# Kernel tuning notes

Measured on AMD Instinct MI355X. Metric: run time of the kernel, lower is better.

Reference implementation:

```python
import jax, jax.numpy as jnp
import numpy as np

def setup_inputs() -> dict:
    key = jax.random.key(0)
    k1, k2 = jax.random.split(key)
    bb_feats = jax.random.normal(k1, (8, 512, 128, 128), dtype=jnp.float32)
    aux_out = jax.random.normal(k2, (8, 19, 128, 128), dtype=jnp.float32)
    return {"bb_feats": bb_feats, "aux_out": aux_out}

def reference(bb_feats, aux_out):
    B, K, H, W = aux_out.shape
    C = bb_feats.shape[1]
    probs = jax.nn.softmax(aux_out.reshape(B, K, H * W), axis=2)  # [B,K,HW]
    feats = bb_feats.reshape(B, C, H * W)                          # [B,C,HW]
    # weighted sum over spatial dim: [B,K,HW] x [B,C,HW] -> [B,K,C]
    ctx = jnp.einsum('bks,bcs->bkc', probs, feats)
    # -> [B,C,K,1]
    return jnp.transpose(ctx, (0, 2, 1))[..., None]
```

## Files before the change

### kernel.cpp

```cpp
#include <hip/hip_runtime.h>
#include <math.h>

#define B 8
#define C 512
#define K 19
#define HW 16384
#define ROWS (B * K)
#define L2E 1.44269504088896340736f

#define NSEG 8
#define SEG (HW / NSEG)

#define NW 4
#define CPW 4
#define CPB (CPW * NW)
#define CG (C / CPB)
#define NSC 4
#define SCHUNK (HW / NSC)
#define TS 256
#define NT (SCHUNK / TS)

__global__ __launch_bounds__(256)
void softmax_partial_kernel(const float* __restrict__ aux, float* __restrict__ partials) {
    int blk = blockIdx.x;
    int row = blk >> 3;
    int seg = blk & (NSEG - 1);
    const float4* x4 = (const float4*)(aux + (size_t)row * HW + seg * SEG);
    int tid  = threadIdx.x;
    int lane = tid & 63;
    int wave = tid >> 6;
    __shared__ float red[4];

    float4 v0 = x4[tid];
    float4 v1 = x4[tid + 256];
    float m = fmaxf(fmaxf(fmaxf(v0.x, v0.y), fmaxf(v0.z, v0.w)),
                    fmaxf(fmaxf(v1.x, v1.y), fmaxf(v1.z, v1.w)));
    #pragma unroll
    for (int off = 32; off > 0; off >>= 1) m = fmaxf(m, __shfl_xor(m, off, 64));
    if (lane == 0) red[wave] = m;
    __syncthreads();
    m = fmaxf(fmaxf(red[0], red[1]), fmaxf(red[2], red[3]));
    __syncthreads();

    float s = exp2f((v0.x - m) * L2E) + exp2f((v0.y - m) * L2E)
            + exp2f((v0.z - m) * L2E) + exp2f((v0.w - m) * L2E)
            + exp2f((v1.x - m) * L2E) + exp2f((v1.y - m) * L2E)
            + exp2f((v1.z - m) * L2E) + exp2f((v1.w - m) * L2E);
    #pragma unroll
    for (int off = 32; off > 0; off >>= 1) s += __shfl_xor(s, off, 64);
    if (lane == 0) red[wave] = s;
    __syncthreads();
    if (tid == 0) {
        partials[blk * 2]     = m;
        partials[blk * 2 + 1] = red[0] + red[1] + red[2] + red[3];
    }
}

__global__ __launch_bounds__(256)
void softmax_combine_kernel(const float* __restrict__ partials, float* __restrict__ stats) {
    int row = threadIdx.x;
    if (row < ROWS) {
        float mj[NSEG], zj[NSEG];
        float m = -INFINITY;
        #pragma unroll
        for (int j = 0; j < NSEG; j++) {
            mj[j] = partials[(row * NSEG + j) * 2];
            zj[j] = partials[(row * NSEG + j) * 2 + 1];
            m = fmaxf(m, mj[j]);
        }
        float Z = 0.f;
        #pragma unroll
        for (int j = 0; j < NSEG; j++) Z += zj[j] * exp2f((mj[j] - m) * L2E);
        stats[row * 2]     = -m * L2E;
        stats[row * 2 + 1] = 1.0f / Z;
    }
}

__global__ __launch_bounds__(256)
__attribute__((amdgpu_waves_per_eu(2)))
void gather_kernel(const float* __restrict__ feats, const float* __restrict__ aux,
                   const float* __restrict__ stats, float* __restrict__ out) {
    __shared__ float plds[2][K][TS];

    int bid  = blockIdx.x;
    int sc   = bid & (NSC - 1);
    int cg   = (bid >> 2) & (CG - 1);
    int b    = bid >> 7;
    int tid  = threadIdx.x;
    int lane = tid & 63;
    int wave = tid >> 6;
    int c0   = cg * CPB + wave * CPW;

    const float* Abase = aux   + (size_t)b * K * HW + sc * SCHUNK;
    const float* Fbase = feats + ((size_t)b * C + c0) * HW + sc * SCHUNK;
    const float* S     = stats + (size_t)b * K * 2;

    float negml[K], invz[K];
    #pragma unroll
    for (int k = 0; k < K; k++) {
        negml[k] = __int_as_float(__builtin_amdgcn_readfirstlane(__float_as_int(S[2 * k])));
        invz[k]  = __int_as_float(__builtin_amdgcn_readfirstlane(__float_as_int(S[2 * k + 1])));
    }

    float acc[CPW][K];
    #pragma unroll
    for (int c = 0; c < CPW; c++)
        #pragma unroll
        for (int k = 0; k < K; k++) acc[c][k] = 0.f;

    #pragma unroll
    for (int k = 0; k < K; k++) {
        float a = Abase[k * HW + tid];
        plds[0][k][tid] = exp2f(fmaf(a, L2E, negml[k])) * invz[k];
    }
    float4 f_cur[CPW], f_next[CPW];
    #pragma unroll
    for (int c = 0; c < CPW; c++)
        f_cur[c] = *(const float4*)(Fbase + c * HW + lane * 4);

    for (int t = 0; t < NT; t++) {
        int buf = t & 1;
        __syncthreads();

        if (t + 1 < NT) {
            int s1 = (t + 1) * TS;
            #pragma unroll
            for (int c = 0; c < CPW; c++)
                f_next[c] = *(const float4*)(Fbase + c * HW + s1 + lane * 4);
            #pragma unroll
            for (int kb = 0; kb < K; kb += 5) {
                float a[5];
                const int ke = (kb + 5 < K) ? kb + 5 : K;
                #pragma unroll
                for (int k = kb; k < ke; k++) a[k - kb] = Abase[k * HW + s1 + tid];
                #pragma unroll
                for (int k = kb; k < ke; k++)
                    plds[buf ^ 1][k][tid] = exp2f(fmaf(a[k - kb], L2E, negml[k])) * invz[k];
            }
        }

        #pragma unroll
        for (int k = 0; k < K; k++) {
            float4 p4 = *(const float4*)(&plds[buf][k][lane * 4]);
            #pragma unroll
            for (int c = 0; c < CPW; c++) {
                acc[c][k] = fmaf(p4.x, f_cur[c].x, acc[c][k]);
                acc[c][k] = fmaf(p4.y, f_cur[c].y, acc[c][k]);
                acc[c][k] = fmaf(p4.z, f_cur[c].z, acc[c][k]);
                acc[c][k] = fmaf(p4.w, f_cur[c].w, acc[c][k]);
            }
        }
        #pragma unroll
        for (int c = 0; c < CPW; c++) f_cur[c] = f_next[c];
    }

    #pragma unroll
    for (int c = 0; c < CPW; c++)
        #pragma unroll
        for (int k = 0; k < K; k++) {
            float v = acc[c][k];
            #pragma unroll
            for (int off = 32; off > 0; off >>= 1) v += __shfl_xor(v, off, 64);
            if (lane == 0)
                atomicAdd(&out[((size_t)b * C + c0 + c) * K + k], v);
        }
}

extern "C" void kernel_launch(void* const* d_in, const int* in_sizes, int n_in,
                              void* d_out, int out_size, void* d_ws, size_t ws_size,
                              hipStream_t stream) {
    const float* feats = (const float*)d_in[0];
    const float* aux   = (const float*)d_in[1];
    float* out      = (float*)d_out;
    float* stats    = (float*)d_ws;
    float* partials = (float*)d_ws + 512;

    hipMemsetAsync(d_out, 0, (size_t)out_size * sizeof(float), stream);
    softmax_partial_kernel<<<ROWS * NSEG, 256, 0, stream>>>(aux, partials);
    softmax_combine_kernel<<<1, 256, 0, stream>>>(partials, stats);
    gather_kernel<<<B * CG * NSC, 256, 0, stream>>>(feats, aux, stats, out);
}
```

Before: 407.2 us.

## Materialize softmax probabilities once and stream them into LDS via direct loads

Replaces the two-stage softmax statistics kernels with one kernel per row that writes fully normalized probabilities to workspace. The gather kernel then loads those probabilities straight into LDS with global_load_lds, which removes the per-block exp recomputation that was repeated for every channel group. It also remaps block IDs so that blocks sharing the same batch and spatial chunk land on the same XCD, aiming for better L2 reuse. In exchange, the probability tensor makes an extra write and read round trip through memory, and the 1024-thread single-row blocks launch only 152 blocks.

Measured after the change: 395.0 us. 3.0% less time.

```diff
diff --git a/kernel.cpp b/kernel.cpp
--- a/kernel.cpp
+++ b/kernel.cpp
@@ -8,9 +8,6 @@
 #define ROWS (B * K)
 #define L2E 1.44269504088896340736f
 
-#define NSEG 8
-#define SEG (HW / NSEG)
-
 #define NW 4
 #define CPW 4
 #define CPB (CPW * NW)
@@ -20,87 +17,85 @@
 #define TS 256
 #define NT (SCHUNK / TS)
 
-__global__ __launch_bounds__(256)
-void softmax_partial_kernel(const float* __restrict__ aux, float* __restrict__ partials) {
-    int blk = blockIdx.x;
-    int row = blk >> 3;
-    int seg = blk & (NSEG - 1);
-    const float4* x4 = (const float4*)(aux + (size_t)row * HW + seg * SEG);
+typedef __attribute__((address_space(3))) unsigned int lds_u32;
+typedef const __attribute__((address_space(1))) unsigned int glb_u32;
+
+__global__ __launch_bounds__(1024)
+void probs_kernel(const float* __restrict__ aux, float* __restrict__ probs) {
+    int row  = blockIdx.x;
     int tid  = threadIdx.x;
     int lane = tid & 63;
     int wave = tid >> 6;
-    __shared__ float red[4];
+    __shared__ float red[16];
 
-    float4 v0 = x4[tid];
-    float4 v1 = x4[tid + 256];
-    float m = fmaxf(fmaxf(fmaxf(v0.x, v0.y), fmaxf(v0.z, v0.w)),
-                    fmaxf(fmaxf(v1.x, v1.y), fmaxf(v1.z, v1.w)));
+    const float4* x4 = (const float4*)(aux + (size_t)row * HW);
+    float4*       p4 = (float4*)(probs + (size_t)row * HW);
+
+    float4 v[4];
+    #pragma unroll
+    for (int i = 0; i < 4; i++) v[i] = x4[tid + i * 1024];
+
+    float m = -INFINITY;
+    #pragma unroll
+    for (int i = 0; i < 4; i++)
+        m = fmaxf(m, fmaxf(fmaxf(v[i].x, v[i].y), fmaxf(v[i].z, v[i].w)));
     #pragma unroll
     for (int off = 32; off > 0; off >>= 1) m = fmaxf(m, __shfl_xor(m, off, 64));
     if (lane == 0) red[wave] = m;
     __syncthreads();
-    m = fmaxf(fmaxf(red[0], red[1]), fmaxf(red[2], red[3]));
+    #pragma unroll
+    for (int w = 0; w < 16; w++) m = fmaxf(m, red[w]);
     __syncthreads();
 
-    float s = exp2f((v0.x - m) * L2E) + exp2f((v0.y - m) * L2E)
-            + exp2f((v0.z - m) * L2E) + exp2f((v0.w - m) * L2E)
-            + exp2f((v1.x - m) * L2E) + exp2f((v1.y - m) * L2E)
-            + exp2f((v1.z - m) * L2E) + exp2f((v1.w - m) * L2E);
+    float nm = -m * L2E;
+    float s = 0.f;
+    #pragma unroll
+    for (int i = 0; i < 4; i++) {
+        v[i].x = exp2f(fmaf(v[i].x, L2E, nm));
+        v[i].y = exp2f(fmaf(v[i].y, L2E, nm));
+        v[i].z = exp2f(fmaf(v[i].z, L2E, nm));
+        v[i].w = exp2f(fmaf(v[i].w, L2E, nm));
+        s += (v[i].x + v[i].y) + (v[i].z + v[i].w);
+    }
     #pragma unroll
     for (int off = 32; off > 0; off >>= 1) s += __shfl_xor(s, off, 64);
     if (lane == 0) red[wave] = s;
     __syncthreads();
-    if (tid == 0) {
-        partials[blk * 2]     = m;
-        partials[blk * 2 + 1] = red[0] + red[1] + red[2] + red[3];
-    }
-}
+    float Z = 0.f;
+    #pragma unroll
+    for (int w = 0; w < 16; w++) Z += red[w];
+    float inv = 1.0f / Z;
 
-__global__ __launch_bounds__(256)
-void softmax_combine_kernel(const float* __restrict__ partials, float* __restrict__ stats) {
-    int row = threadIdx.x;
-    if (row < ROWS) {
-        float mj[NSEG], zj[NSEG];
-        float m = -INFINITY;
-        #pragma unroll
-        for (int j = 0; j < NSEG; j++) {
-            mj[j] = partials[(row * NSEG + j) * 2];
-            zj[j] = partials[(row * NSEG + j) * 2 + 1];
-            m = fmaxf(m, mj[j]);
-        }
-        float Z = 0.f;
-        #pragma unroll
-        for (int j = 0; j < NSEG; j++) Z += zj[j] * exp2f((mj[j] - m) * L2E);
-        stats[row * 2]     = -m * L2E;
-        stats[row * 2 + 1] = 1.0f / Z;
+    #pragma unroll
+    for (int i = 0; i < 4; i++) {
+        float4 o;
+        o.x = v[i].x * inv; o.y = v[i].y * inv;
+        o.z = v[i].z * inv; o.w = v[i].w * inv;
+        p4[tid + i * 1024] = o;
     }
 }
 
 __global__ __launch_bounds__(256)
 __attribute__((amdgpu_waves_per_eu(2)))
-void gather_kernel(const float* __restrict__ feats, const float* __restrict__ aux,
-                   const float* __restrict__ stats, float* __restrict__ out) {
+void gather_kernel(const float* __restrict__ feats, const float* __restrict__ probs,
+                   float* __restrict__ out) {
     __shared__ float plds[2][K][TS];
 
-    int bid  = blockIdx.x;
-    int sc   = bid & (NSC - 1);
-    int cg   = (bid >> 2) & (CG - 1);
-    int b    = bid >> 7;
+    int bid = blockIdx.x;
+    int xcd = bid & 7;
+    int lid = xcd * 128 + (bid >> 3);
+    int cg  = lid & (CG - 1);
+    int grp = lid >> 5;
+    int sc  = grp & (NSC - 1);
+    int b   = grp >> 2;
+
     int tid  = threadIdx.x;
     int lane = tid & 63;
     int wave = tid >> 6;
     int c0   = cg * CPB + wave * CPW;
 
-    const float* Abase = aux   + (size_t)b * K * HW + sc * SCHUNK;
+    const float* Pbase = probs + (size_t)b * K * HW + sc * SCHUNK;
     const float* Fbase = feats + ((size_t)b * C + c0) * HW + sc * SCHUNK;
-    const float* S     = stats + (size_t)b * K * 2;
-
-    float negml[K], invz[K];
-    #pragma unroll
-    for (int k = 0; k < K; k++) {
-        negml[k] = __int_as_float(__builtin_amdgcn_readfirstlane(__float_as_int(S[2 * k])));
-        invz[k]  = __int_as_float(__builtin_amdgcn_readfirstlane(__float_as_int(S[2 * k + 1])));
-    }
 
     float acc[CPW][K];
     #pragma unroll
@@ -108,11 +103,9 @@
         #pragma unroll
         for (int k = 0; k < K; k++) acc[c][k] = 0.f;
 
-    #pragma unroll
-    for (int k = 0; k < K; k++) {
-        float a = Abase[k * HW + tid];
-        plds[0][k][tid] = exp2f(fmaf(a, L2E, negml[k])) * invz[k];
-    }
+    for (int k = wave; k < K; k += NW)
+        __builtin_amdgcn_global_load_lds((glb_u32*)(Pbase + (size_t)k * HW + lane * 4),
+                                         (lds_u32*)&plds[0][k][0], 16, 0, 0);
     float4 f_cur[CPW], f_next[CPW];
     #pragma unroll
     for (int c = 0; c < CPW; c++)
@@ -127,27 +120,20 @@
             #pragma unroll
             for (int c = 0; c < CPW; c++)
                 f_next[c] = *(const float4*)(Fbase + c * HW + s1 + lane * 4);
-            #pragma unroll
-            for (int kb = 0; kb < K; kb += 5) {
-                float a[5];
-                const int ke = (kb + 5 < K) ? kb + 5 : K;
-                #pragma unroll
-                for (int k = kb; k < ke; k++) a[k - kb] = Abase[k * HW + s1 + tid];
-                #pragma unroll
-                for (int k = kb; k < ke; k++)
-                    plds[buf ^ 1][k][tid] = exp2f(fmaf(a[k - kb], L2E, negml[k])) * invz[k];
-            }
+            for (int k = wave; k < K; k += NW)
+                __builtin_amdgcn_global_load_lds((glb_u32*)(Pbase + (size_t)k * HW + s1 + lane * 4),
+                                                 (lds_u32*)&plds[buf ^ 1][k][0], 16, 0, 0);
         }
 
         #pragma unroll
         for (int k = 0; k < K; k++) {
-            float4 p4 = *(const float4*)(&plds[buf][k][lane * 4]);
+            float4 pv = *(const float4*)(&plds[buf][k][lane * 4]);
             #pragma unroll
             for (int c = 0; c < CPW; c++) {
-                acc[c][k] = fmaf(p4.x, f_cur[c].x, acc[c][k]);
-                acc[c][k] = fmaf(p4.y, f_cur[c].y, acc[c][k]);
-                acc[c][k] = fmaf(p4.z, f_cur[c].z, acc[c][k]);
-                acc[c][k] = fmaf(p4.w, f_cur[c].w, acc[c][k]);
+                acc[c][k] = fmaf(pv.x, f_cur[c].x, acc[c][k]);
+                acc[c][k] = fmaf(pv.y, f_cur[c].y, acc[c][k]);
+                acc[c][k] = fmaf(pv.z, f_cur[c].z, acc[c][k]);
+                acc[c][k] = fmaf(pv.w, f_cur[c].w, acc[c][k]);
             }
         }
         #pragma unroll
@@ -171,12 +157,10 @@
                               hipStream_t stream) {
     const float* feats = (const float*)d_in[0];
     const float* aux   = (const float*)d_in[1];
-    float* out      = (float*)d_out;
-    float* stats    = (float*)d_ws;
-    float* partials = (float*)d_ws + 512;
+    float* out   = (float*)d_out;
+    float* probs = (float*)d_ws;
 
     hipMemsetAsync(d_out, 0, (size_t)out_size * sizeof(float), stream);
-    softmax_partial_kernel<<<ROWS * NSEG, 256, 0, stream>>>(aux, partials);
-    softmax_combine_kernel<<<1, 256, 0, stream>>>(partials, stats);
-    gather_kernel<<<B * CG * NSC, 256, 0, stream>>>(feats, aux, stats, out);
+    probs_kernel<<<ROWS, 1024, 0, stream>>>(aux, probs);
+    gather_kernel<<<B * CG * NSC, 256, 0, stream>>>(feats, probs, out);
 }
```
